# Kernel optimization log

Hardware: AMD Instinct MI355X
Metric: run time of the kernel (lower is better)

The kernel has to match this reference:

```python
import jax, jax.numpy as jnp
import numpy as np

NUM_HEADS = 8
LN_EPS = 1e-5


def _layernorm(t, w, b):
    mu = t.mean(-1, keepdims=True)
    var = t.var(-1, keepdims=True)  # ddof=0, matches torch LayerNorm
    return (t - mu) * jax.lax.rsqrt(var + LN_EPS) * w + b


def setup_inputs() -> dict:
    key = jax.random.key(0)
    ks = jax.random.split(key, 5)
    B, C, H, W = 16, 384, 32, 32
    hidden = 4 * C
    s = 0.02
    return {
        "x": jax.random.normal(ks[0], (B, C, H, W), jnp.float32),
        "ln1_w": jnp.ones((C,), jnp.float32),
        "ln1_b": jnp.zeros((C,), jnp.float32),
        "qkv_w": s * jax.random.normal(ks[1], (3 * C, C), jnp.float32),
        "qkv_b": jnp.zeros((3 * C,), jnp.float32),
        "proj_w": s * jax.random.normal(ks[2], (C, C), jnp.float32),
        "proj_b": jnp.zeros((C,), jnp.float32),
        "ln2_w": jnp.ones((C,), jnp.float32),
        "ln2_b": jnp.zeros((C,), jnp.float32),
        "fc1_w": s * jax.random.normal(ks[3], (hidden, C), jnp.float32),
        "fc1_b": jnp.zeros((hidden,), jnp.float32),
        "fc2_w": s * jax.random.normal(ks[4], (C, hidden), jnp.float32),
        "fc2_b": jnp.zeros((C,), jnp.float32),
    }


def reference(x, ln1_w, ln1_b, qkv_w, qkv_b, proj_w, proj_b,
              ln2_w, ln2_b, fc1_w, fc1_b, fc2_w, fc2_b):
    B, C, H, W = x.shape
    N = H * W
    nh = NUM_HEADS
    hd = C // nh
    scale = hd ** (-0.5)

    xf = x.reshape(B, C, N).transpose(0, 2, 1)  # (B, N, C) tokens

    # --- pre-norm attention ---
    h1 = _layernorm(xf, ln1_w, ln1_b)
    qkv = h1 @ qkv_w.T + qkv_b                      # (B, N, 3C)
    qkv = qkv.reshape(B, N, 3, nh, hd).transpose(2, 0, 3, 1, 4)  # (3,B,h,N,d)
    q, k, v = qkv[0], qkv[1], qkv[2]
    attn = jax.nn.softmax(jnp.einsum('bhnd,bhmd->bhnm', q, k) * scale, axis=-1)
    out = jnp.einsum('bhnm,bhmd->bhnd', attn, v)    # (B,h,N,d)
    out = out.transpose(0, 2, 1, 3).reshape(B, N, C)
    out = out @ proj_w.T + proj_b
    xf = xf + out

    # --- pre-norm FFN (exact GELU, matching torch nn.GELU default) ---
    h2 = _layernorm(xf, ln2_w, ln2_b)
    f = jax.nn.gelu(h2 @ fc1_w.T + fc1_b, approximate=False)
    f = f @ fc2_w.T + fc2_b
    xf = xf + f

    return xf.transpose(0, 2, 1).reshape(B, C, H, W)
```

## Files before the change

### kernel.cpp

```cpp
#include <hip/hip_runtime.h>

typedef unsigned short u16;
using bf16x8 = __attribute__((ext_vector_type(8))) short;
using f32x4  = __attribute__((ext_vector_type(4))) float;

#define DEV __device__ __forceinline__

constexpr int    NTOK = 16384;
constexpr size_t QKSZ = (size_t)16 * 8 * 1024 * 64;
constexpr float  ATTN_SCALE = 0.14433756729740645f;

DEV u16 f2bf(float x) {
  unsigned int u = __float_as_uint(x);
  u += 0x7fffu + ((u >> 16) & 1u);
  return (u16)(u >> 16);
}

DEV void async16(const u16* g, u16* l) {
  __builtin_amdgcn_global_load_lds(
      (const __attribute__((address_space(1))) unsigned int*)g,
      (__attribute__((address_space(3))) unsigned int*)l, 16, 0, 0);
}

DEV const bf16x8* lds_swz(const u16* base, int row, int bytecol) {
  int byte = row * 128 + bytecol;
  byte ^= (row & 7) << 4;
  return (const bf16x8*)((const char*)base + byte);
}

DEV float gelu_f(float x) {
  float y = 0.7978845608028654f * (x + 0.044715f * x * x * x);
  float e = __expf(2.f * y);
  float t = 1.f - 2.f / (e + 1.f);
  return 0.5f * x * (1.f + t);
}

__global__ void cvt_kernel(const float* __restrict__ qkvw, const float* __restrict__ qkvb,
                           const float* __restrict__ projw, const float* __restrict__ fc1w,
                           const float* __restrict__ fc2w,
                           u16* __restrict__ wqkvp, float* __restrict__ biasp,
                           u16* __restrict__ wproj, u16* __restrict__ wfc1,
                           u16* __restrict__ wfc2) {
  int i = blockIdx.x * 256 + threadIdx.x;
  if (i < 147456) {
    int p = i / 96, q = (i - p * 96) * 4;
    int which = p >> 9, h = (p >> 6) & 7, d = p & 63;
    ushort4 o{0, 0, 0, 0};
    if (d < 48) {
      float sc = which ? 1.f : ATTN_SCALE;
      float4 v = *(const float4*)(qkvw + (size_t)(which * 384 + h * 48 + d) * 384 + q);
      o = ushort4{f2bf(v.x * sc), f2bf(v.y * sc), f2bf(v.z * sc), f2bf(v.w * sc)};
    }
    *(ushort4*)(wqkvp + (size_t)p * 384 + q) = o;
  } else if (i < 479232) {
    const float* s; u16* d; int off;
    if (i < 184320)      { s = projw; d = wproj; off = i - 147456; }
    else if (i < 331776) { s = fc1w;  d = wfc1;  off = i - 184320; }
    else                 { s = fc2w;  d = wfc2;  off = i - 331776; }
    float4 v = *(const float4*)(s + (size_t)off * 4);
    *(ushort4*)(d + (size_t)off * 4) = ushort4{f2bf(v.x), f2bf(v.y), f2bf(v.z), f2bf(v.w)};
  } else if (i < 479616) {
    int qi = (i - 479232) * 4;
    float4 o;
    float* op = (float*)&o;
#pragma unroll
    for (int r = 0; r < 4; ++r) {
      int p = qi + r, which = p >> 9, h = (p >> 6) & 7, d = p & 63;
      op[r] = (d < 48) ? qkvb[which * 384 + h * 48 + d] * (which ? 1.f : ATTN_SCALE) : 0.f;
    }
    *(float4*)(biasp + qi) = o;
  }
}

__global__ __launch_bounds__(256) void ln_kernel(
    const float* __restrict__ in, const float* __restrict__ gw,
    const float* __restrict__ gb, u16* __restrict__ out) {
  __shared__ float tile[32][385];
  __shared__ float mu_s[32], rs_s[32];
  const int b = blockIdx.y;
  const int n0 = blockIdx.x * 32;
  const int t = threadIdx.x;
  const int j = t & 31, cb = t >> 5;
  const float* src = in + (size_t)b * 384 * 1024 + n0;
  for (int k = 0; k < 48; ++k) {
    int c = k * 8 + cb;
    tile[j][c] = src[(size_t)c * 1024 + j];
  }
  __syncthreads();
  const int jt = t >> 3, r = t & 7;
  float s = 0.f, ss = 0.f;
  for (int c = r; c < 384; c += 8) { float v = tile[jt][c]; s += v; ss += v * v; }
  s += __shfl_xor(s, 1); ss += __shfl_xor(ss, 1);
  s += __shfl_xor(s, 2); ss += __shfl_xor(ss, 2);
  s += __shfl_xor(s, 4); ss += __shfl_xor(ss, 4);
  const float mean = s * (1.f / 384.f);
  const float var  = ss * (1.f / 384.f) - mean * mean;
  if (r == 0) { mu_s[jt] = mean; rs_s[jt] = rsqrtf(var + 1e-5f); }
  __syncthreads();
  for (int q = t; q < 3072; q += 256) {
    int tok = q / 96, c4 = (q - tok * 96) * 4;
    float m = mu_s[tok], rv = rs_s[tok];
    float4 wv = *(const float4*)(gw + c4);
    float4 bv = *(const float4*)(gb + c4);
    u16* dst = out + (size_t)(b * 1024 + n0 + tok) * 384 + c4;
    ushort4 o{f2bf((tile[tok][c4 + 0] - m) * rv * wv.x + bv.x),
              f2bf((tile[tok][c4 + 1] - m) * rv * wv.y + bv.y),
              f2bf((tile[tok][c4 + 2] - m) * rv * wv.z + bv.z),
              f2bf((tile[tok][c4 + 3] - m) * rv * wv.w + bv.w)};
    *(ushort4*)dst = o;
  }
}

template<int EPI>
__global__ __launch_bounds__(512, 2) void gemm256_kernel(
    const u16* __restrict__ A, const u16* __restrict__ W,
    const float* __restrict__ bias, u16* __restrict__ outh, int K) {
  __shared__ u16 sA[2][16384], sB[2][16384];
  const int m0 = blockIdx.x * 256, n0 = blockIdx.y * 256;
  const int tid = threadIdx.x;
  const int wv = tid >> 6, lane = tid & 63;
  const int wm = (wv >> 2) * 128, wn = (wv & 3) * 64;
  const int l16 = lane & 15, lg = lane >> 4;
  const int ksw = (l16 & 7) << 4;

  f32x4 acc[8][4];
#pragma unroll
  for (int i = 0; i < 8; ++i)
#pragma unroll
    for (int jj = 0; jj < 4; ++jj) acc[i][jj] = f32x4{0.f, 0.f, 0.f, 0.f};

  const int nk = K >> 6;
  auto stage = [&](int buf, int kt) {
    const u16* Ab = A + (size_t)m0 * K + kt * 64;
    const u16* Wb = W + (size_t)n0 * K + kt * 64;
#pragma unroll
    for (int j = 0; j < 4; ++j) {
      int cb = j * 512 + wv * 64;
      int c = cb + lane;
      int row = c >> 3, sl = (c & 7) ^ (row & 7);
      async16(Ab + (size_t)row * K + sl * 8, &sA[buf][cb * 8]);
      async16(Wb + (size_t)row * K + sl * 8, &sB[buf][cb * 8]);
    }
  };
  stage(0, 0);
  int buf = 0;
  for (int kt = 0; kt < nk; ++kt) {
    asm volatile("s_waitcnt vmcnt(0)" ::: "memory");
    __builtin_amdgcn_s_barrier();
    if (kt + 1 < nk) stage(buf ^ 1, kt + 1);
#pragma unroll
    for (int ks = 0; ks < 2; ++ks) {
      bf16x8 av[8], bv[4];
#pragma unroll
      for (int f = 0; f < 4; ++f) {
        int rb = wn + f * 16 + l16;
        bv[f] = *(const bf16x8*)((const char*)&sB[buf][0] + rb * 128 + ((ks * 64 + lg * 16) ^ ksw));
      }
#pragma unroll
      for (int f = 0; f < 8; ++f) {
        int ra = wm + f * 16 + l16;
        av[f] = *(const bf16x8*)((const char*)&sA[buf][0] + ra * 128 + ((ks * 64 + lg * 16) ^ ksw));
      }
      __builtin_amdgcn_s_setprio(1);
#pragma unroll
      for (int mf = 0; mf < 8; ++mf)
#pragma unroll
        for (int nf = 0; nf < 4; ++nf)
          acc[mf][nf] = __builtin_amdgcn_mfma_f32_16x16x32_bf16(bv[nf], av[mf], acc[mf][nf], 0, 0, 0);
      __builtin_amdgcn_s_setprio(0);
    }
    buf ^= 1;
  }

#pragma unroll
  for (int mf = 0; mf < 8; ++mf) {
    const int token = m0 + wm + mf * 16 + l16;
    const int b = token >> 10, nn = token & 1023;
#pragma unroll
    for (int nf = 0; nf < 4; ++nf) {
      const int col = n0 + wn + nf * 16 + lg * 4;
      f32x4 v = acc[mf][nf];
      float4 bb = *(const float4*)(bias + col);
      unsigned long long pk = 0;
      if constexpr (EPI == 0) {
#pragma unroll
        for (int rr = 0; rr < 4; ++rr)
          pk |= (unsigned long long)f2bf(v[rr] + ((const float*)&bb)[rr]) << (16 * rr);
        const int which = col >> 9, h = (col >> 6) & 7, d0 = col & 63;
        size_t idx = (size_t)which * QKSZ + (size_t)((b * 8 + h) * 1024 + nn) * 64 + d0;
        *(unsigned long long*)&outh[idx] = pk;
      } else {
#pragma unroll
        for (int rr = 0; rr < 4; ++rr)
          pk |= (unsigned long long)f2bf(gelu_f(v[rr] + ((const float*)&bb)[rr])) << (16 * rr);
        *(unsigned long long*)&outh[(size_t)token * 1536 + col] = pk;
      }
    }
  }
}

template<int EPI>
__global__ __launch_bounds__(256, 2) void gemm_kernel(
    const u16* __restrict__ A, const u16* __restrict__ W,
    const float* __restrict__ bias, float* __restrict__ outf,
    u16* __restrict__ outh, const float* __restrict__ resid, int K) {
  __shared__ u16 sA[2][8192], sB[2][8192];
  const int m0 = blockIdx.x * 128;
  const int n0 = (EPI == 4 ? 1024 : 0) + blockIdx.y * 128;
  const int wv = threadIdx.x >> 6, lane = threadIdx.x & 63;
  const int wm = (wv >> 1) * 64, wn = (wv & 1) * 64;
  const int l16 = lane & 15, lg = lane >> 4;
  const int ksw = (l16 & 7) << 4;

  f32x4 acc[4][4];
#pragma unroll
  for (int i = 0; i < 4; ++i)
#pragma unroll
    for (int jj = 0; jj < 4; ++jj) acc[i][jj] = f32x4{0.f, 0.f, 0.f, 0.f};

  const int nk = K >> 6;
  auto stage = [&](int buf, int kt) {
    const u16* Ab = A + (size_t)m0 * K + kt * 64;
    const u16* Wb = W + (size_t)n0 * K + kt * 64;
#pragma unroll
    for (int j = 0; j < 4; ++j) {
      int cb = j * 256 + wv * 64;
      int c = cb + lane;
      int row = c >> 3, sl = (c & 7) ^ (row & 7);
      async16(Ab + (size_t)row * K + sl * 8, &sA[buf][cb * 8]);
      async16(Wb + (size_t)row * K + sl * 8, &sB[buf][cb * 8]);
    }
  };
  stage(0, 0);
  int buf = 0;
  for (int kt = 0; kt < nk; ++kt) {
    asm volatile("s_waitcnt vmcnt(0)" ::: "memory");
    __builtin_amdgcn_s_barrier();
    if (kt + 1 < nk) stage(buf ^ 1, kt + 1);
#pragma unroll
    for (int ks = 0; ks < 2; ++ks) {
      bf16x8 av[4], bv[4];
#pragma unroll
      for (int f = 0; f < 4; ++f) {
        int ra = wm + f * 16 + l16, rb = wn + f * 16 + l16;
        av[f] = *(const bf16x8*)((const char*)&sA[buf][0] + ra * 128 + ((ks * 64 + lg * 16) ^ ksw));
        bv[f] = *(const bf16x8*)((const char*)&sB[buf][0] + rb * 128 + ((ks * 64 + lg * 16) ^ ksw));
      }
      __builtin_amdgcn_s_setprio(1);
#pragma unroll
      for (int mf = 0; mf < 4; ++mf)
#pragma unroll
        for (int nf = 0; nf < 4; ++nf)
          acc[mf][nf] = __builtin_amdgcn_mfma_f32_16x16x32_bf16(av[mf], bv[nf], acc[mf][nf], 0, 0, 0);
      __builtin_amdgcn_s_setprio(0);
    }
    buf ^= 1;
  }

#pragma unroll
  for (int mf = 0; mf < 4; ++mf) {
    const int mm = m0 + wm + mf * 16 + lg * 4;
    const int b = mm >> 10, nn = mm & 1023;
#pragma unroll
    for (int nf = 0; nf < 4; ++nf) {
      const int col = n0 + wn + nf * 16 + l16;
      f32x4 v = acc[mf][nf];
      const float bs = bias[col];
      if constexpr (EPI == 4) {
        unsigned long long pk = 0;
#pragma unroll
        for (int rr = 0; rr < 4; ++rr)
          pk |= (unsigned long long)f2bf(v[rr] + bs) << (16 * rr);
        const int h = (col >> 6) & 7, d = col & 63;
        size_t idx = 2ull * QKSZ + (((size_t)((b * 8 + h) * 64 + d)) << 10) + nn;
        *(unsigned long long*)&outh[idx] = pk;
      } else {
        size_t idx = ((size_t)(b * 384 + col) << 10) + nn;
        float4 rr4 = *(const float4*)&resid[idx];
        float4 o{v[0] + bs + rr4.x, v[1] + bs + rr4.y, v[2] + bs + rr4.z, v[3] + bs + rr4.w};
        *(float4*)&outf[idx] = o;
      }
    }
  }
}

__global__ __launch_bounds__(256, 3) void attn_kernel(
    const u16* __restrict__ Qg, const u16* __restrict__ Kg,
    const u16* __restrict__ Vtg, u16* __restrict__ outp) {
  __shared__ u16 Ks[2][4096];
  __shared__ u16 Vs[2][4096];
  __shared__ u16 QPs[4 * 32 * 72];
  const int orig = blockIdx.x;
  const int swz = (orig & 7) * 128 + (orig >> 3);
  const int bh = swz >> 3, qt = swz & 7;
  const int w = threadIdx.x >> 6, lane = threadIdx.x & 63;
  const int l16 = lane & 15, lg = lane >> 4;

  const u16* kbase = Kg + (size_t)bh * 1024 * 64;
  const u16* vbase = Vtg + (size_t)bh * 64 * 1024;

  auto stageKV = [&](int buf, int kv) {
#pragma unroll
    for (int i = 0; i < 2; ++i) {
      int cb = (i * 4 + w) * 64;
      int ck = cb + lane;
      int g  = ck ^ ((ck >> 3) & 7);
      async16(kbase + (size_t)kv * 4096 + g * 8, &Ks[buf][cb * 8]);
      async16(vbase + (size_t)(g >> 3) * 1024 + kv * 64 + (g & 7) * 8, &Vs[buf][cb * 8]);
    }
  };

  {
    const u16* src = Qg + (size_t)(bh * 1024 + qt * 128) * 64;
#pragma unroll
    for (int i = 0; i < 4; ++i) {
      int cb = (i * 4 + w) * 64;
      int ck = cb + lane;
      int g  = ck ^ ((ck >> 3) & 7);
      async16(src + g * 8, &QPs[cb * 8]);
    }
  }
  stageKV(0, 0);
  asm volatile("s_waitcnt vmcnt(0)" ::: "memory");
  __builtin_amdgcn_s_barrier();

  bf16x8 qf[2][2];
#pragma unroll
  for (int mf = 0; mf < 2; ++mf)
#pragma unroll
    for (int ks = 0; ks < 2; ++ks)
      qf[mf][ks] = *lds_swz(QPs, w * 32 + mf * 16 + l16, ks * 64 + lg * 16);
  asm volatile("s_waitcnt lgkmcnt(0)" ::: "memory");
  __builtin_amdgcn_s_barrier();

  float lr[2][4];
  f32x4 acco[2][4];
#pragma unroll
  for (int mf = 0; mf < 2; ++mf) {
#pragma unroll
    for (int r = 0; r < 4; ++r) lr[mf][r] = 0.f;
#pragma unroll
    for (int df = 0; df < 4; ++df) acco[mf][df] = f32x4{0.f, 0.f, 0.f, 0.f};
  }
  u16* Pw = &QPs[w * 32 * 72];

  auto compute = [&](int buf) {
    f32x4 accs[2][4];
#pragma unroll
    for (int mf = 0; mf < 2; ++mf)
#pragma unroll
      for (int nf = 0; nf < 4; ++nf) accs[mf][nf] = f32x4{0.f, 0.f, 0.f, 0.f};
    __builtin_amdgcn_s_setprio(1);
#pragma unroll
    for (int nf = 0; nf < 4; ++nf) {
      bf16x8 k0 = *lds_swz(Ks[buf], nf * 16 + l16, lg * 16);
      bf16x8 k1 = *lds_swz(Ks[buf], nf * 16 + l16, 64 + lg * 16);
#pragma unroll
      for (int mf = 0; mf < 2; ++mf) {
        accs[mf][nf] = __builtin_amdgcn_mfma_f32_16x16x32_bf16(qf[mf][0], k0, accs[mf][nf], 0, 0, 0);
        accs[mf][nf] = __builtin_amdgcn_mfma_f32_16x16x32_bf16(qf[mf][1], k1, accs[mf][nf], 0, 0, 0);
      }
    }
    __builtin_amdgcn_s_setprio(0);
#pragma unroll
    for (int mf = 0; mf < 2; ++mf)
#pragma unroll
      for (int r = 0; r < 4; ++r) {
        float s0 = __expf(accs[mf][0][r]);
        float s1 = __expf(accs[mf][1][r]);
        float s2 = __expf(accs[mf][2][r]);
        float s3 = __expf(accs[mf][3][r]);
        accs[mf][0][r] = s0; accs[mf][1][r] = s1;
        accs[mf][2][r] = s2; accs[mf][3][r] = s3;
        lr[mf][r] += s0 + s1 + s2 + s3;
      }
#pragma unroll
    for (int mf = 0; mf < 2; ++mf)
#pragma unroll
      for (int nf = 0; nf < 4; ++nf)
#pragma unroll
        for (int r = 0; r < 4; ++r)
          Pw[(mf * 16 + lg * 4 + r) * 72 + nf * 16 + l16] = f2bf(accs[mf][nf][r]);
    asm volatile("s_waitcnt lgkmcnt(0)" ::: "memory");
#pragma unroll
    for (int ks = 0; ks < 2; ++ks) {
      bf16x8 pa[2], vf[4];
#pragma unroll
      for (int mf = 0; mf < 2; ++mf)
        pa[mf] = *(const bf16x8*)&Pw[(mf * 16 + l16) * 72 + ks * 32 + lg * 8];
#pragma unroll
      for (int df = 0; df < 4; ++df)
        vf[df] = *lds_swz(Vs[buf], df * 16 + l16, ks * 64 + lg * 16);
      __builtin_amdgcn_s_setprio(1);
#pragma unroll
      for (int mf = 0; mf < 2; ++mf)
#pragma unroll
        for (int df = 0; df < 4; ++df)
          acco[mf][df] = __builtin_amdgcn_mfma_f32_16x16x32_bf16(pa[mf], vf[df], acco[mf][df], 0, 0, 0);
      __builtin_amdgcn_s_setprio(0);
    }
  };

  int buf = 0;
  for (int kv = 0; kv < 16; ++kv) {
    if (kv + 1 < 16) stageKV(buf ^ 1, kv + 1);
    compute(buf);
    asm volatile("s_waitcnt vmcnt(0)" ::: "memory");
    __builtin_amdgcn_s_barrier();
    buf ^= 1;
  }

  const int b = bh >> 3, h = bh & 7;
#pragma unroll
  for (int mf = 0; mf < 2; ++mf)
#pragma unroll
    for (int r = 0; r < 4; ++r) {
      float t = lr[mf][r];
      t += __shfl_xor(t, 1); t += __shfl_xor(t, 2);
      t += __shfl_xor(t, 4); t += __shfl_xor(t, 8);
      float inv = 1.f / t;
      int token = qt * 128 + w * 32 + mf * 16 + lg * 4 + r;
      size_t rowb = (size_t)(b * 1024 + token) * 384 + h * 48;
#pragma unroll
      for (int df = 0; df < 3; ++df)
        outp[rowb + df * 16 + l16] = f2bf(acco[mf][df][r] * inv);
    }
}

constexpr size_t OFF_WQKVP = 0;
constexpr size_t OFF_BIASP = 1179648;
constexpr size_t OFF_WPROJ = 1185792;
constexpr size_t OFF_WFC1  = 1480704;
constexpr size_t OFF_WFC2  = 2660352;
constexpr size_t OFF_H     = 3840000;
constexpr size_t OFF_QKV   = 16422912;
constexpr size_t OFF_AO    = 66754560;
constexpr size_t OFF_Y1T   = 79337472;

extern "C" void kernel_launch(void* const* d_in, const int* in_sizes, int n_in,
                              void* d_out, int out_size, void* d_ws, size_t ws_size,
                              hipStream_t stream) {
  (void)in_sizes; (void)n_in; (void)out_size; (void)ws_size;
  const float* x     = (const float*)d_in[0];
  const float* ln1w  = (const float*)d_in[1];
  const float* ln1b  = (const float*)d_in[2];
  const float* qkvw  = (const float*)d_in[3];
  const float* qkvbi = (const float*)d_in[4];
  const float* projw = (const float*)d_in[5];
  const float* projb = (const float*)d_in[6];
  const float* ln2w  = (const float*)d_in[7];
  const float* ln2b  = (const float*)d_in[8];
  const float* fc1w  = (const float*)d_in[9];
  const float* fc1b  = (const float*)d_in[10];
  const float* fc2w  = (const float*)d_in[11];
  const float* fc2b  = (const float*)d_in[12];

  char* ws = (char*)d_ws;
  u16*   wqkvp = (u16*)(ws + OFF_WQKVP);
  float* biasp = (float*)(ws + OFF_BIASP);
  u16*   wproj = (u16*)(ws + OFF_WPROJ);
  u16*   wfc1  = (u16*)(ws + OFF_WFC1);
  u16*   wfc2  = (u16*)(ws + OFF_WFC2);
  u16*   h1    = (u16*)(ws + OFF_H);
  u16*   qkvs  = (u16*)(ws + OFF_QKV);
  u16*   f1    = qkvs;
  u16*   ao    = (u16*)(ws + OFF_AO);
  float* y1t   = (float*)(ws + OFF_Y1T);

  cvt_kernel<<<1874, 256, 0, stream>>>(qkvw, qkvbi, projw, fc1w, fc2w,
                                       wqkvp, biasp, wproj, wfc1, wfc2);

  dim3 lngrid(32, 16);
  ln_kernel<<<lngrid, 256, 0, stream>>>(x, ln1w, ln1b, h1);

  gemm256_kernel<0><<<dim3(64, 4), 512, 0, stream>>>(h1, wqkvp, biasp, qkvs, 384);
  gemm_kernel<4><<<dim3(128, 4), 256, 0, stream>>>(h1, wqkvp, biasp, nullptr, qkvs, nullptr, 384);

  attn_kernel<<<dim3(1024), 256, 0, stream>>>(qkvs, qkvs + QKSZ, qkvs + 2 * QKSZ, ao);

  gemm_kernel<1><<<dim3(128, 3), 256, 0, stream>>>(ao, wproj, projb, y1t, nullptr, x, 384);

  ln_kernel<<<lngrid, 256, 0, stream>>>(y1t, ln2w, ln2b, h1 );

  gemm256_kernel<2><<<dim3(64, 6), 512, 0, stream>>>(h1, wfc1, fc1b, f1, 384);

  gemm_kernel<3><<<dim3(128, 3), 256, 0, stream>>>(f1, wfc2, fc2b, (float*)d_out, nullptr, y1t, 1536);
}
```

Measured before the change: 317.7 us.

## Rework attention with 32x32 MFMA and register P, XCD-remap GEMMs, halve K tile

The attention kernel now computes S transposed with 32x32x16 MFMAs and keeps the exponentiated P in registers. It packs P with cvt_pk_bf16 and permlane32_swap instead of round-tripping it through LDS, which removes a shared-memory write/read and a wait per KV tile. The GEMM kernels remap block indices so neighbouring tiles share an XCD for better L2 reuse. The 256-tile GEMM halves its K step to 32 with a new swizzle, cutting LDS use so more blocks can be resident, at the cost of more barriers per K.

```diff
diff --git a/kernel.cpp b/kernel.cpp
--- a/kernel.cpp
+++ b/kernel.cpp
@@ -3,6 +3,7 @@
 typedef unsigned short u16;
 using bf16x8 = __attribute__((ext_vector_type(8))) short;
 using f32x4  = __attribute__((ext_vector_type(4))) float;
+using f32x16 = __attribute__((ext_vector_type(16))) float;
 
 #define DEV __device__ __forceinline__
 
@@ -26,6 +27,13 @@
   int byte = row * 128 + bytecol;
   byte ^= (row & 7) << 4;
   return (const bf16x8*)((const char*)base + byte);
+}
+
+DEV f32x16 zero16() {
+  f32x16 z;
+#pragma unroll
+  for (int i = 0; i < 16; ++i) z[i] = 0.f;
+  return z;
 }
 
 DEV float gelu_f(float x) {
@@ -33,6 +41,14 @@
   float e = __expf(2.f * y);
   float t = 1.f - 2.f / (e + 1.f);
   return 0.5f * x * (1.f + t);
+}
+
+DEV void xcd_remap(int& bx, int& by) {
+  int p = blockIdx.x + gridDim.x * blockIdx.y;
+  int nxs = gridDim.x >> 3;
+  int xcd = p & 7, q = p >> 3;
+  bx = xcd * nxs + q % nxs;
+  by = q / nxs;
 }
 
 __global__ void cvt_kernel(const float* __restrict__ qkvw, const float* __restrict__ qkvb,
@@ -115,13 +131,14 @@
 __global__ __launch_bounds__(512, 2) void gemm256_kernel(
     const u16* __restrict__ A, const u16* __restrict__ W,
     const float* __restrict__ bias, u16* __restrict__ outh, int K) {
-  __shared__ u16 sA[2][16384], sB[2][16384];
-  const int m0 = blockIdx.x * 256, n0 = blockIdx.y * 256;
+  __shared__ u16 sA[2][8192], sB[2][8192];
+  int bx, by; xcd_remap(bx, by);
+  const int m0 = bx * 256, n0 = by * 256;
   const int tid = threadIdx.x;
   const int wv = tid >> 6, lane = tid & 63;
   const int wm = (wv >> 2) * 128, wn = (wv & 3) * 64;
   const int l16 = lane & 15, lg = lane >> 4;
-  const int ksw = (l16 & 7) << 4;
+  const int rsw = ((lg ^ (l16 & 3)) << 4);
 
   f32x4 acc[8][4];
 #pragma unroll
@@ -129,15 +146,15 @@
 #pragma unroll
     for (int jj = 0; jj < 4; ++jj) acc[i][jj] = f32x4{0.f, 0.f, 0.f, 0.f};
 
-  const int nk = K >> 6;
+  const int nk = K >> 5;
   auto stage = [&](int buf, int kt) {
-    const u16* Ab = A + (size_t)m0 * K + kt * 64;
-    const u16* Wb = W + (size_t)n0 * K + kt * 64;
-#pragma unroll
-    for (int j = 0; j < 4; ++j) {
+    const u16* Ab = A + (size_t)m0 * K + kt * 32;
+    const u16* Wb = W + (size_t)n0 * K + kt * 32;
+#pragma unroll
+    for (int j = 0; j < 2; ++j) {
       int cb = j * 512 + wv * 64;
       int c = cb + lane;
-      int row = c >> 3, sl = (c & 7) ^ (row & 7);
+      int row = c >> 2, sl = (c & 3) ^ (row & 3);
       async16(Ab + (size_t)row * K + sl * 8, &sA[buf][cb * 8]);
       async16(Wb + (size_t)row * K + sl * 8, &sB[buf][cb * 8]);
     }
@@ -148,27 +165,20 @@
     asm volatile("s_waitcnt vmcnt(0)" ::: "memory");
     __builtin_amdgcn_s_barrier();
     if (kt + 1 < nk) stage(buf ^ 1, kt + 1);
-#pragma unroll
-    for (int ks = 0; ks < 2; ++ks) {
-      bf16x8 av[8], bv[4];
-#pragma unroll
-      for (int f = 0; f < 4; ++f) {
-        int rb = wn + f * 16 + l16;
-        bv[f] = *(const bf16x8*)((const char*)&sB[buf][0] + rb * 128 + ((ks * 64 + lg * 16) ^ ksw));
-      }
-#pragma unroll
-      for (int f = 0; f < 8; ++f) {
-        int ra = wm + f * 16 + l16;
-        av[f] = *(const bf16x8*)((const char*)&sA[buf][0] + ra * 128 + ((ks * 64 + lg * 16) ^ ksw));
-      }
-      __builtin_amdgcn_s_setprio(1);
-#pragma unroll
-      for (int mf = 0; mf < 8; ++mf)
-#pragma unroll
-        for (int nf = 0; nf < 4; ++nf)
-          acc[mf][nf] = __builtin_amdgcn_mfma_f32_16x16x32_bf16(bv[nf], av[mf], acc[mf][nf], 0, 0, 0);
-      __builtin_amdgcn_s_setprio(0);
-    }
+    bf16x8 av[8], bv[4];
+#pragma unroll
+    for (int f = 0; f < 4; ++f)
+      bv[f] = *(const bf16x8*)((const char*)&sB[buf][0] + (wn + f * 16 + l16) * 64 + rsw);
+#pragma unroll
+    for (int f = 0; f < 8; ++f)
+      av[f] = *(const bf16x8*)((const char*)&sA[buf][0] + (wm + f * 16 + l16) * 64 + rsw);
+    __builtin_amdgcn_s_setprio(1);
+#pragma unroll
+    for (int mf = 0; mf < 8; ++mf)
+#pragma unroll
+      for (int nf = 0; nf < 4; ++nf)
+        acc[mf][nf] = __builtin_amdgcn_mfma_f32_16x16x32_bf16(bv[nf], av[mf], acc[mf][nf], 0, 0, 0);
+    __builtin_amdgcn_s_setprio(0);
     buf ^= 1;
   }
 
@@ -205,8 +215,9 @@
     const float* __restrict__ bias, float* __restrict__ outf,
     u16* __restrict__ outh, const float* __restrict__ resid, int K) {
   __shared__ u16 sA[2][8192], sB[2][8192];
-  const int m0 = blockIdx.x * 128;
-  const int n0 = (EPI == 4 ? 1024 : 0) + blockIdx.y * 128;
+  int bx, by; xcd_remap(bx, by);
+  const int m0 = bx * 128;
+  const int n0 = (EPI == 4 ? 1024 : 0) + by * 128;
   const int wv = threadIdx.x >> 6, lane = threadIdx.x & 63;
   const int wm = (wv >> 1) * 64, wn = (wv & 1) * 64;
   const int l16 = lane & 15, lg = lane >> 4;
@@ -289,15 +300,15 @@
     const u16* __restrict__ Vtg, u16* __restrict__ outp) {
   __shared__ u16 Ks[2][4096];
   __shared__ u16 Vs[2][4096];
-  __shared__ u16 QPs[4 * 32 * 72];
+  __shared__ u16 Qs[8192];
   const int orig = blockIdx.x;
   const int swz = (orig & 7) * 128 + (orig >> 3);
   const int bh = swz >> 3, qt = swz & 7;
   const int w = threadIdx.x >> 6, lane = threadIdx.x & 63;
-  const int l16 = lane & 15, lg = lane >> 4;
-
-  const u16* kbase = Kg + (size_t)bh * 1024 * 64;
-  const u16* vbase = Vtg + (size_t)bh * 64 * 1024;
+  const int l31 = lane & 31, hi = lane >> 5;
+
+  const u16* kbase = Kg + (size_t)bh * 65536;
+  const u16* vbase = Vtg + (size_t)bh * 65536;
 
   auto stageKV = [&](int buf, int kv) {
 #pragma unroll
@@ -317,114 +328,90 @@
       int cb = (i * 4 + w) * 64;
       int ck = cb + lane;
       int g  = ck ^ ((ck >> 3) & 7);
-      async16(src + g * 8, &QPs[cb * 8]);
+      async16(src + g * 8, &Qs[cb * 8]);
     }
   }
   stageKV(0, 0);
   asm volatile("s_waitcnt vmcnt(0)" ::: "memory");
   __builtin_amdgcn_s_barrier();
 
-  bf16x8 qf[2][2];
-#pragma unroll
-  for (int mf = 0; mf < 2; ++mf)
-#pragma unroll
-    for (int ks = 0; ks < 2; ++ks)
-      qf[mf][ks] = *lds_swz(QPs, w * 32 + mf * 16 + l16, ks * 64 + lg * 16);
-  asm volatile("s_waitcnt lgkmcnt(0)" ::: "memory");
-  __builtin_amdgcn_s_barrier();
-
-  float lr[2][4];
-  f32x4 acco[2][4];
-#pragma unroll
-  for (int mf = 0; mf < 2; ++mf) {
-#pragma unroll
-    for (int r = 0; r < 4; ++r) lr[mf][r] = 0.f;
-#pragma unroll
-    for (int df = 0; df < 4; ++df) acco[mf][df] = f32x4{0.f, 0.f, 0.f, 0.f};
-  }
-  u16* Pw = &QPs[w * 32 * 72];
-
-  auto compute = [&](int buf) {
-    f32x4 accs[2][4];
-#pragma unroll
-    for (int mf = 0; mf < 2; ++mf)
-#pragma unroll
-      for (int nf = 0; nf < 4; ++nf) accs[mf][nf] = f32x4{0.f, 0.f, 0.f, 0.f};
-    __builtin_amdgcn_s_setprio(1);
-#pragma unroll
-    for (int nf = 0; nf < 4; ++nf) {
-      bf16x8 k0 = *lds_swz(Ks[buf], nf * 16 + l16, lg * 16);
-      bf16x8 k1 = *lds_swz(Ks[buf], nf * 16 + l16, 64 + lg * 16);
-#pragma unroll
-      for (int mf = 0; mf < 2; ++mf) {
-        accs[mf][nf] = __builtin_amdgcn_mfma_f32_16x16x32_bf16(qf[mf][0], k0, accs[mf][nf], 0, 0, 0);
-        accs[mf][nf] = __builtin_amdgcn_mfma_f32_16x16x32_bf16(qf[mf][1], k1, accs[mf][nf], 0, 0, 0);
-      }
-    }
-    __builtin_amdgcn_s_setprio(0);
-#pragma unroll
-    for (int mf = 0; mf < 2; ++mf)
-#pragma unroll
-      for (int r = 0; r < 4; ++r) {
-        float s0 = __expf(accs[mf][0][r]);
-        float s1 = __expf(accs[mf][1][r]);
-        float s2 = __expf(accs[mf][2][r]);
-        float s3 = __expf(accs[mf][3][r]);
-        accs[mf][0][r] = s0; accs[mf][1][r] = s1;
-        accs[mf][2][r] = s2; accs[mf][3][r] = s3;
-        lr[mf][r] += s0 + s1 + s2 + s3;
-      }
-#pragma unroll
-    for (int mf = 0; mf < 2; ++mf)
-#pragma unroll
-      for (int nf = 0; nf < 4; ++nf)
-#pragma unroll
-        for (int r = 0; r < 4; ++r)
-          Pw[(mf * 16 + lg * 4 + r) * 72 + nf * 16 + l16] = f2bf(accs[mf][nf][r]);
-    asm volatile("s_waitcnt lgkmcnt(0)" ::: "memory");
-#pragma unroll
-    for (int ks = 0; ks < 2; ++ks) {
-      bf16x8 pa[2], vf[4];
-#pragma unroll
-      for (int mf = 0; mf < 2; ++mf)
-        pa[mf] = *(const bf16x8*)&Pw[(mf * 16 + l16) * 72 + ks * 32 + lg * 8];
-#pragma unroll
-      for (int df = 0; df < 4; ++df)
-        vf[df] = *lds_swz(Vs[buf], df * 16 + l16, ks * 64 + lg * 16);
-      __builtin_amdgcn_s_setprio(1);
-#pragma unroll
-      for (int mf = 0; mf < 2; ++mf)
-#pragma unroll
-        for (int df = 0; df < 4; ++df)
-          acco[mf][df] = __builtin_amdgcn_mfma_f32_16x16x32_bf16(pa[mf], vf[df], acco[mf][df], 0, 0, 0);
-      __builtin_amdgcn_s_setprio(0);
-    }
-  };
+  bf16x8 qf[4];
+#pragma unroll
+  for (int ds = 0; ds < 4; ++ds)
+    qf[ds] = *lds_swz(Qs, w * 32 + l31, ds * 32 + hi * 16);
+
+  f32x16 out0 = zero16(), out1 = zero16();
+  float ls0 = 0.f, ls1 = 0.f;
 
   int buf = 0;
   for (int kv = 0; kv < 16; ++kv) {
     if (kv + 1 < 16) stageKV(buf ^ 1, kv + 1);
-    compute(buf);
+
+    f32x16 sacc0 = zero16(), sacc1 = zero16();
+    __builtin_amdgcn_s_setprio(1);
+#pragma unroll
+    for (int ds = 0; ds < 4; ++ds) {
+      bf16x8 kf0 = *lds_swz(Ks[buf], l31,      ds * 32 + hi * 16);
+      bf16x8 kf1 = *lds_swz(Ks[buf], 32 + l31, ds * 32 + hi * 16);
+      sacc0 = __builtin_amdgcn_mfma_f32_32x32x16_bf16(kf0, qf[ds], sacc0, 0, 0, 0);
+      sacc1 = __builtin_amdgcn_mfma_f32_32x32x16_bf16(kf1, qf[ds], sacc1, 0, 0, 0);
+    }
+    __builtin_amdgcn_s_setprio(0);
+
+    unsigned int c0[8], c1[8];
+#pragma unroll
+    for (int i = 0; i < 8; ++i) {
+      float a = __expf(sacc0[2 * i]), b = __expf(sacc0[2 * i + 1]);
+      ls0 += a + b;
+      unsigned int pk;
+      asm("v_cvt_pk_bf16_f32 %0, %1, %2" : "=v"(pk) : "v"(a), "v"(b));
+      c0[i] = pk;
+    }
+#pragma unroll
+    for (int i = 0; i < 8; ++i) {
+      float a = __expf(sacc1[2 * i]), b = __expf(sacc1[2 * i + 1]);
+      ls1 += a + b;
+      unsigned int pk;
+      asm("v_cvt_pk_bf16_f32 %0, %1, %2" : "=v"(pk) : "v"(a), "v"(b));
+      c1[i] = pk;
+    }
+
+#pragma unroll
+    for (int m = 0; m < 4; ++m) {
+      unsigned int a0 = (m < 2) ? c0[(m & 1) * 4 + 0] : c1[(m & 1) * 4 + 0];
+      unsigned int b0 = (m < 2) ? c0[(m & 1) * 4 + 2] : c1[(m & 1) * 4 + 2];
+      unsigned int a1 = (m < 2) ? c0[(m & 1) * 4 + 1] : c1[(m & 1) * 4 + 1];
+      unsigned int b1 = (m < 2) ? c0[(m & 1) * 4 + 3] : c1[(m & 1) * 4 + 3];
+      asm volatile("v_permlane32_swap_b32 %0, %1" : "+v"(a0), "+v"(b0));
+      asm volatile("v_permlane32_swap_b32 %0, %1" : "+v"(a1), "+v"(b1));
+      union { int4 i; bf16x8 v; } u;
+      u.i = int4{(int)a0, (int)a1, (int)b0, (int)b1};
+      bf16x8 pa = u.v;
+      bf16x8 v0 = *lds_swz(Vs[buf], l31,      m * 32 + hi * 16);
+      bf16x8 v1 = *lds_swz(Vs[buf], 32 + l31, m * 32 + hi * 16);
+      __builtin_amdgcn_s_setprio(1);
+      out0 = __builtin_amdgcn_mfma_f32_32x32x16_bf16(pa, v0, out0, 0, 0, 0);
+      out1 = __builtin_amdgcn_mfma_f32_32x32x16_bf16(pa, v1, out1, 0, 0, 0);
+      __builtin_amdgcn_s_setprio(0);
+    }
+
     asm volatile("s_waitcnt vmcnt(0)" ::: "memory");
     __builtin_amdgcn_s_barrier();
     buf ^= 1;
   }
 
+  float lf = ls0 + ls1;
+  lf += __shfl_xor(lf, 32);
   const int b = bh >> 3, h = bh & 7;
 #pragma unroll
-  for (int mf = 0; mf < 2; ++mf)
-#pragma unroll
-    for (int r = 0; r < 4; ++r) {
-      float t = lr[mf][r];
-      t += __shfl_xor(t, 1); t += __shfl_xor(t, 2);
-      t += __shfl_xor(t, 4); t += __shfl_xor(t, 8);
-      float inv = 1.f / t;
-      int token = qt * 128 + w * 32 + mf * 16 + lg * 4 + r;
-      size_t rowb = (size_t)(b * 1024 + token) * 384 + h * 48;
-#pragma unroll
-      for (int df = 0; df < 3; ++df)
-        outp[rowb + df * 16 + l16] = f2bf(acco[mf][df][r] * inv);
-    }
+  for (int r = 0; r < 16; ++r) {
+    const int q = (r & 3) + 8 * (r >> 2) + 4 * hi;
+    const float inv = 1.f / __shfl(lf, q);
+    const int token = qt * 128 + w * 32 + q;
+    const size_t rowb = (size_t)(b * 1024 + token) * 384 + h * 48;
+    outp[rowb + l31] = f2bf(out0[r] * inv);
+    if (l31 < 16) outp[rowb + 32 + l31] = f2bf(out1[r] * inv);
+  }
 }
 
 constexpr size_t OFF_WQKVP = 0;
```

Result: no change. 315.0 us (-0.8%).
